# Optimization experiments

Hardware: AMD Instinct MI355X
Metric: run time of the kernel (lower is better)

The kernel has to match this reference:

```python
import jax, jax.numpy as jnp
import numpy as np

E = 8            # n_expert
K = 2            # n_expert_per_token
C = 2048         # n_embd
I = 1408         # moe_intermediate_size
IS = I * 2       # shared expert intermediate (n_shared_expert=2)
B, T = 2, 2048


def setup_inputs() -> dict:
    key = jax.random.key(0)
    ks = jax.random.split(key, 9)
    s = 0.02
    return {
        "x": jax.random.normal(ks[0], (B, T, C), dtype=jnp.float32),
        "gate_w": jax.random.normal(ks[1], (E, C), dtype=jnp.float32) * s,
        # expert MLP weights, torch Linear convention (out_features, in_features)
        "w1": jax.random.normal(ks[2], (E, I, C), dtype=jnp.float32) * s,  # fc_1
        "w2": jax.random.normal(ks[3], (E, I, C), dtype=jnp.float32) * s,  # fc_2
        "w3": jax.random.normal(ks[4], (E, C, I), dtype=jnp.float32) * s,  # proj
        # shared expert
        "sw1": jax.random.normal(ks[5], (IS, C), dtype=jnp.float32) * s,
        "sw2": jax.random.normal(ks[6], (IS, C), dtype=jnp.float32) * s,
        "sw3": jax.random.normal(ks[7], (C, IS), dtype=jnp.float32) * s,
    }


def reference(x, gate_w, w1, w2, w3, sw1, sw2, sw3):
    Bq, Tq, Cq = x.shape
    xf = x.reshape(-1, Cq)  # [N, C], N = B*T

    # top-k routing: softmax in fp32, then top-k probs per token
    logits = xf @ gate_w.T                                   # [N, E]
    probs = jax.nn.softmax(logits.astype(jnp.float32), axis=-1)
    topk_p, topk_i = jax.lax.top_k(probs, K)                 # [N, K]
    # combine weights: comb[n, e] = sum_k topk_p[n,k] * (topk_i[n,k] == e)
    comb = (jax.nn.one_hot(topk_i, E, dtype=jnp.float32)
            * topk_p[..., None]).sum(axis=1).astype(x.dtype)  # [N, E]

    # per-expert gated-SiLU MLP (batched over experts via einsum)
    h1 = jnp.einsum('nc,eic->eni', xf, w1)                   # [E, N, I]
    h2 = jnp.einsum('nc,eic->eni', xf, w2)                   # [E, N, I]
    h = jax.nn.silu(h1) * h2
    eo = jnp.einsum('eni,eci->enc', h, w3)                   # [E, N, C]

    # weighted scatter-combine
    y = jnp.einsum('enc,ne->nc', eo, comb).reshape(Bq, Tq, Cq)

    # shared expert on the residual input
    sh = (jax.nn.silu(xf @ sw1.T) * (xf @ sw2.T)) @ sw3.T    # [N, C]
    return y + sh.reshape(Bq, Tq, Cq)
```

## Files before the change

### kernel.cpp

```cpp
#include <hip/hip_runtime.h>
#include <stdint.h>

#define N_TOK 4096
#define CDIM  2048
#define NEXP  8
#define IDIM  1408
#define ISDIM 2816
#define CAP   2048
#define ICAT  2816
#define SCAT  5632

typedef __attribute__((ext_vector_type(8))) short bf16x8;
typedef __attribute__((ext_vector_type(4))) float f32x4;

#define GLOAD16(gp, lp) __builtin_amdgcn_global_load_lds( \
    (const __attribute__((address_space(1))) void*)(gp),  \
    (__attribute__((address_space(3))) void*)(lp), 16, 0, 0)

__device__ __forceinline__ unsigned short f2bf(float f) {
  union { float f; unsigned u; } c; c.f = f;
  return (unsigned short)((c.u + 0x7FFFu + ((c.u >> 16) & 1u)) >> 16);
}
__device__ __forceinline__ float bf2f(unsigned short h) {
  union { unsigned u; float f; } c; c.u = (unsigned)h << 16;
  return c.f;
}

__device__ __forceinline__ int xcd_swizzle(int orig, int nwg) {
  int q = nwg >> 3, r = nwg & 7;
  int xcd = orig & 7, idx = orig >> 3;
  return (xcd < r ? xcd * (q + 1) : r * (q + 1) + (xcd - r) * q) + idx;
}

__global__ __launch_bounds__(256) void cvt_all(
    const float* __restrict__ x, const float* __restrict__ w1,
    const float* __restrict__ w2, const float* __restrict__ w3,
    const float* __restrict__ sw1, const float* __restrict__ sw2,
    const float* __restrict__ sw3,
    unsigned short* __restrict__ xb, unsigned short* __restrict__ wcat,
    unsigned short* __restrict__ w3b, unsigned short* __restrict__ swcat,
    unsigned short* __restrict__ sw3b) {
  const int b = blockIdx.x;
  const int t = threadIdx.x;
  const float* src;
  unsigned short* dst;
  if (b < 4096) {
    src = x + (size_t)b * 2048;  dst = xb + (size_t)b * 2048;
  } else if (b < 15360) {
    size_t o = (size_t)(b - 4096) * 2048;  src = w3 + o;  dst = w3b + o;
  } else if (b < 18176) {
    size_t o = (size_t)(b - 15360) * 2048; src = sw3 + o; dst = sw3b + o;
  } else if (b < 40704) {
    int g = b - 18176;
    int e = g / 2816, r = g - e * 2816;
    int dr;
    if (r < 1408) { src = w1 + ((size_t)e * 1408 + r) * 2048; dr = (r >> 7) * 256 + (r & 127); }
    else { int r2 = r - 1408; src = w2 + ((size_t)e * 1408 + r2) * 2048; dr = (r2 >> 7) * 256 + 128 + (r2 & 127); }
    dst = wcat + ((size_t)e * ICAT + dr) * 2048;
  } else {
    int g = b - 40704;
    int dr;
    if (g < 2816) {
      int zn = g >= 1408, rr = g - zn * 1408;
      src = sw1 + (size_t)g * 2048;
      dr = zn * 2816 + (rr >> 7) * 256 + (rr & 127);
    } else {
      int r = g - 2816;
      int zn = r >= 1408, rr = r - zn * 1408;
      src = sw2 + (size_t)r * 2048;
      dr = zn * 2816 + (rr >> 7) * 256 + 128 + (rr & 127);
    }
    dst = swcat + (size_t)dr * 2048;
  }
  size_t i = (size_t)t * 8;
  float4 v0 = *(const float4*)(src + i);
  float4 v1 = *(const float4*)(src + i + 4);
  bf16x8 o;
  o[0] = (short)f2bf(v0.x); o[1] = (short)f2bf(v0.y);
  o[2] = (short)f2bf(v0.z); o[3] = (short)f2bf(v0.w);
  o[4] = (short)f2bf(v1.x); o[5] = (short)f2bf(v1.y);
  o[6] = (short)f2bf(v1.z); o[7] = (short)f2bf(v1.w);
  *(bf16x8*)(dst + i) = o;
}

__global__ __launch_bounds__(64) void routing_kernel(
    const float* __restrict__ x, const float* __restrict__ gw,
    int* __restrict__ counts, int* __restrict__ list,
    int* __restrict__ slot_of, float* __restrict__ wts) {
  const int n = blockIdx.x;
  const int lane = threadIdx.x;
  const float* xr = x + (size_t)n * CDIM;
  float s[NEXP];
#pragma unroll
  for (int e = 0; e < NEXP; e++) s[e] = 0.f;
  for (int c = lane; c < CDIM; c += 64) {
    float xv = xr[c];
#pragma unroll
    for (int e = 0; e < NEXP; e++) s[e] += xv * gw[e * CDIM + c];
  }
#pragma unroll
  for (int e = 0; e < NEXP; e++) {
    float v = s[e];
    for (int o = 32; o > 0; o >>= 1) v += __shfl_down(v, o);
    s[e] = v;
  }
  if (lane == 0) {
    float mx = s[0];
#pragma unroll
    for (int e = 1; e < NEXP; e++) mx = fmaxf(mx, s[e]);
    float p[NEXP], sum = 0.f;
#pragma unroll
    for (int e = 0; e < NEXP; e++) { p[e] = __expf(s[e] - mx); sum += p[e]; }
    int i0 = 0;
#pragma unroll
    for (int e = 1; e < NEXP; e++) if (p[e] > p[i0]) i0 = e;
    int i1 = (i0 == 0) ? 1 : 0;
#pragma unroll
    for (int e = 0; e < NEXP; e++) if (e != i0 && p[e] > p[i1]) i1 = e;
    float inv = 1.f / sum;
    int s0 = atomicAdd(&counts[i0], 1);
    int s1 = atomicAdd(&counts[i1], 1);
    if (s0 < CAP) list[i0 * CAP + s0] = n; else s0 = 0;
    if (s1 < CAP) list[i1 * CAP + s1] = n; else s1 = 0;
    slot_of[n * 2]     = i0 * CAP + s0;
    slot_of[n * 2 + 1] = i1 * CAP + s1;
    wts[n * 2]     = p[i0] * inv;
    wts[n * 2 + 1] = p[i1] * inv;
  }
}

template <int PHASE>
__global__ __launch_bounds__(512, 2) void moe_gemm(
    const unsigned short* __restrict__ xb,
    const unsigned short* __restrict__ swcat,
    const unsigned short* __restrict__ wcat,
    unsigned short* __restrict__ hs_out,
    unsigned short* __restrict__ he_out,
    const unsigned short* __restrict__ hs,
    const unsigned short* __restrict__ sw3b,
    const unsigned short* __restrict__ he,
    const unsigned short* __restrict__ w3b,
    float* __restrict__ ysf,
    unsigned short* __restrict__ eo,
    const int* __restrict__ list,
    const int* __restrict__ counts) {
  const int z = blockIdx.z;
  const unsigned short *A, *B;
  unsigned short* O = nullptr;
  float* Of = nullptr;
  int Ka, ldo;
  int cnt = 1 << 30;
  const int* lst = nullptr;
  int Mt, Nt;
  bool gath = false;
  if (PHASE == 1) {
    Mt = 16; Ka = CDIM;
    if (z < 2) {
      Nt = 22;
      A = xb + (size_t)z * 2048 * CDIM;
      B = swcat;
      O = hs_out + (size_t)z * 2048 * ISDIM;
      ldo = ISDIM;
    } else {
      Nt = 11;
      int e = z - 2;
      cnt = counts[e]; if (cnt > CAP) cnt = CAP;
      lst = list + e * CAP;
      gath = true;
      A = xb;
      B = wcat + (size_t)e * ICAT * CDIM;
      O = he_out + (size_t)e * CAP * IDIM;
      ldo = IDIM;
    }
  } else {
    Mt = 16; Nt = 8;
    if (z < 2) {
      Ka = ISDIM;
      A = hs + (size_t)z * 2048 * ISDIM;
      B = sw3b;
      Of = ysf + (size_t)z * 2048 * CDIM;
      ldo = CDIM;
    } else {
      int e = z - 2;
      cnt = counts[e]; if (cnt > CAP) cnt = CAP;
      Ka = IDIM;
      A = he + (size_t)e * CAP * IDIM;
      B = w3b + (size_t)e * CDIM * IDIM;
      O = eo + (size_t)e * CAP * CDIM;
      ldo = CDIM;
    }
  }
  const int nwg = Mt * Nt;
  if ((int)blockIdx.x >= nwg) return;
  const int wg = xcd_swizzle(blockIdx.x, nwg);
  const int mt = wg % Mt, nt = wg / Mt;
  if (mt * 128 >= cnt) return;

  __shared__ __align__(16) char lds[2][24576];

  const int tid = threadIdx.x;
  const int srow = tid >> 2;
  const int c16  = (tid & 3) << 4;
  const int scol = c16 ^ (((srow >> 1) & 3) << 4);
  const char* aS;
  const char* bS[2];
  {
    int ar = mt * 128 + srow;
    if (PHASE == 1 && gath) ar = (ar < cnt) ? lst[ar] : lst[0];
    aS = (const char*)A + (size_t)ar * Ka * 2 + scol;
    bS[0] = (const char*)B + (size_t)(nt * 256 + srow) * Ka * 2 + scol;
    bS[1] = (const char*)B + (size_t)(nt * 256 + 128 + srow) * Ka * 2 + scol;
  }
  auto stage = [&](int buf, int kt) {
    size_t kb = (size_t)kt * 64;
    char* d = &lds[buf][0] + tid * 16;
    GLOAD16(aS + kb, d);
    GLOAD16(bS[0] + kb, d + 8192);
    GLOAD16(bS[1] + kb, d + 16384);
  };

  const int lane = tid & 63, wid = tid >> 6;
  const int wr = wid >> 2, wc = wid & 3;
  const int lrow = lane & 15;
  const int klane = (lane >> 4) << 4;
  const int rsw = ((lrow >> 1) & 3) << 4;
  const int aOff = (wr * 64 + lrow) * 64 + (klane ^ rsw);
  const int bOff = 8192 + (wc * 64 + lrow) * 64 + (klane ^ rsw);

  f32x4 acc[4][4];
#pragma unroll
  for (int mf = 0; mf < 4; mf++)
#pragma unroll
    for (int nf = 0; nf < 4; nf++) acc[mf][nf] = (f32x4){0.f, 0.f, 0.f, 0.f};

  stage(0, 0);
  stage(1, 1);

  const int ntk = Ka >> 5;
  for (int t = 0; t < ntk; t++) {
    const char* base = lds[t & 1];
    if (t + 1 < ntk) asm volatile("s_waitcnt vmcnt(3)" ::: "memory");
    else             asm volatile("s_waitcnt vmcnt(0)" ::: "memory");
    __builtin_amdgcn_s_barrier();
    bf16x8 aR[4], bR[4];
#pragma unroll
    for (int i = 0; i < 4; i++) aR[i] = *(const bf16x8*)(base + aOff + i * 1024);
#pragma unroll
    for (int i = 0; i < 4; i++) bR[i] = *(const bf16x8*)(base + bOff + i * 1024);
    asm volatile("s_waitcnt lgkmcnt(0)" ::: "memory");
    __builtin_amdgcn_s_barrier();
    if (t + 2 < ntk) stage(t & 1, t + 2);
    __builtin_amdgcn_s_setprio(1);
#pragma unroll
    for (int nf = 0; nf < 4; nf++)
#pragma unroll
      for (int mf = 0; mf < 4; mf++)
        acc[mf][nf] = __builtin_amdgcn_mfma_f32_16x16x32_bf16(
            aR[mf], bR[nf], acc[mf][nf], 0, 0, 0);
    __builtin_amdgcn_s_setprio(0);
  }

  const int r4 = (lane >> 4) * 4;
  if (PHASE == 1) {
    unsigned short* ldsH = (unsigned short*)&lds[0][0];
    if (wc >= 2) {
      const int cb = (wc - 2) * 64;
#pragma unroll
      for (int mf = 0; mf < 4; mf++)
#pragma unroll
        for (int nf = 0; nf < 4; nf++) {
          int cc = cb + nf * 16 + lrow;
#pragma unroll
          for (int r = 0; r < 4; r++) {
            int rr = wr * 64 + mf * 16 + r4 + r;
            ldsH[rr * 128 + (cc ^ (((rr >> 2) & 7) << 4))] = f2bf(acc[mf][nf][r]);
          }
        }
    }
    __syncthreads();
    if (wc < 2) {
      const int cb = wc * 64;
#pragma unroll
      for (int mf = 0; mf < 4; mf++) {
#pragma unroll
        for (int nf = 0; nf < 4; nf++) {
          int cc = cb + nf * 16 + lrow;
          int col = nt * 128 + cc;
#pragma unroll
          for (int r = 0; r < 4; r++) {
            int rr = wr * 64 + mf * 16 + r4 + r;
            float z1 = acc[mf][nf][r];
            float z2 = bf2f(ldsH[rr * 128 + (cc ^ (((rr >> 2) & 7) << 4))]);
            float gv = z1 / (1.f + __expf(-z1)) * z2;
            O[(size_t)(mt * 128 + rr) * ldo + col] = f2bf(gv);
          }
        }
      }
    }
  } else {
    const int rowb = mt * 128 + wr * 64;
    const int colb = nt * 256 + wc * 64;
#pragma unroll
    for (int mf = 0; mf < 4; mf++) {
      int row0 = rowb + mf * 16 + r4;
#pragma unroll
      for (int nf = 0; nf < 4; nf++) {
        int col = colb + nf * 16 + lrow;
#pragma unroll
        for (int r = 0; r < 4; r++) {
          if (z < 2)
            Of[(size_t)(row0 + r) * ldo + col] = acc[mf][nf][r];
          else
            O[(size_t)(row0 + r) * ldo + col] = f2bf(acc[mf][nf][r]);
        }
      }
    }
  }
}

__global__ __launch_bounds__(256) void combine_kernel(
    float* __restrict__ y, const float* __restrict__ ysf,
    const unsigned short* __restrict__ eo,
    const int* __restrict__ slot_of, const float* __restrict__ wts) {
  int idx = blockIdx.x * 256 + threadIdx.x;
  int n = idx >> 9;
  int c = (idx & 511) * 4;
  float4 v = *(const float4*)(ysf + (size_t)n * CDIM + c);
#pragma unroll
  for (int k = 0; k < 2; k++) {
    int slot = slot_of[n * 2 + k];
    float w = wts[n * 2 + k];
    ushort4 h = *(const ushort4*)(eo + (size_t)slot * CDIM + c);
    v.x += w * bf2f(h.x);
    v.y += w * bf2f(h.y);
    v.z += w * bf2f(h.z);
    v.w += w * bf2f(h.w);
  }
  *(float4*)(y + (size_t)n * CDIM + c) = v;
}

extern "C" void kernel_launch(void* const* d_in, const int* in_sizes, int n_in,
                              void* d_out, int out_size, void* d_ws, size_t ws_size,
                              hipStream_t stream) {
  const float* x   = (const float*)d_in[0];
  const float* gw  = (const float*)d_in[1];
  const float* w1  = (const float*)d_in[2];
  const float* w2  = (const float*)d_in[3];
  const float* w3  = (const float*)d_in[4];
  const float* sw1 = (const float*)d_in[5];
  const float* sw2 = (const float*)d_in[6];
  const float* sw3 = (const float*)d_in[7];
  float* y = (float*)d_out;

  char* ws = (char*)d_ws;
  size_t off = 0;
  auto alloc = [&](size_t b) -> void* {
    void* p = ws + off;
    off += (b + 255) & ~(size_t)255;
    return p;
  };
  unsigned short* xb    = (unsigned short*)alloc((size_t)N_TOK * CDIM * 2);
  unsigned short* wcat  = (unsigned short*)alloc((size_t)NEXP * ICAT * CDIM * 2);
  unsigned short* w3b   = (unsigned short*)alloc((size_t)NEXP * CDIM * IDIM * 2);
  unsigned short* swcat = (unsigned short*)alloc((size_t)SCAT * CDIM * 2);
  unsigned short* sw3b  = (unsigned short*)alloc((size_t)CDIM * ISDIM * 2);
  unsigned short* hs    = (unsigned short*)alloc((size_t)N_TOK * ISDIM * 2);
  unsigned short* he    = (unsigned short*)alloc((size_t)NEXP * CAP * IDIM * 2);
  float*          ysf   = (float*)alloc((size_t)N_TOK * CDIM * 4);
  int*   counts  = (int*)alloc(NEXP * 4);
  int*   list    = (int*)alloc((size_t)NEXP * CAP * 4);
  int*   slot_of = (int*)alloc((size_t)N_TOK * 2 * 4);
  float* wtsb    = (float*)alloc((size_t)N_TOK * 2 * 4);
  unsigned short* eoB = wcat;

  hipMemsetAsync(counts, 0, NEXP * 4, stream);
  routing_kernel<<<N_TOK, 64, 0, stream>>>(x, gw, counts, list, slot_of, wtsb);

  cvt_all<<<46336, 256, 0, stream>>>(x, w1, w2, w3, sw1, sw2, sw3,
                                     xb, wcat, w3b, swcat, sw3b);

  moe_gemm<1><<<dim3(352, 1, 10), 512, 0, stream>>>(
      xb, swcat, wcat, hs, he, hs, sw3b, he, w3b, ysf, eoB, list, counts);

  moe_gemm<2><<<dim3(128, 1, 10), 512, 0, stream>>>(
      xb, swcat, wcat, hs, he, hs, sw3b, he, w3b, ysf, eoB, list, counts);

  combine_kernel<<<(N_TOK * (CDIM / 4)) / 256, 256, 0, stream>>>(y, ysf, eoB, slot_of, wtsb);
}
```

Measured before the change: 633.2 us.

## Enlarge GEMM tiles to 256x256 with triple-buffered LDS pipeline

Doubles the M tile of both MoE GEMM phases from 128 to 256 rows, so each workgroup holds 8x4 MFMA accumulators per wave and reuses each B tile across twice as many rows. It also switches LDS staging from double to triple buffering, which removes the second barrier per k-step, and splits the shared-expert phase-1 work into four z-slices instead of two. This halves the number of A/B tile reloads and the sync overhead. In exchange it drops the occupancy hint from 2 to 1 workgroup per CU, raises register pressure, uses 96KB of LDS, and launches fewer workgroups, which may underfill the GPU, especially for lightly loaded experts.

```diff
diff --git a/kernel.cpp b/kernel.cpp
--- a/kernel.cpp
+++ b/kernel.cpp
@@ -130,7 +130,7 @@
 }
 
 template <int PHASE>
-__global__ __launch_bounds__(512, 2) void moe_gemm(
+__global__ __launch_bounds__(512) void moe_gemm(
     const unsigned short* __restrict__ xb,
     const unsigned short* __restrict__ swcat,
     const unsigned short* __restrict__ wcat,
@@ -154,16 +154,15 @@
   int Mt, Nt;
   bool gath = false;
   if (PHASE == 1) {
-    Mt = 16; Ka = CDIM;
-    if (z < 2) {
-      Nt = 22;
-      A = xb + (size_t)z * 2048 * CDIM;
-      B = swcat;
-      O = hs_out + (size_t)z * 2048 * ISDIM;
+    Mt = 8; Nt = 11; Ka = CDIM;
+    if (z < 4) {
+      int zm = z >> 1, zn = z & 1;
+      A = xb + (size_t)zm * 2048 * CDIM;
+      B = swcat + (size_t)zn * 2816 * CDIM;
+      O = hs_out + (size_t)zm * 2048 * ISDIM + (size_t)zn * 1408;
       ldo = ISDIM;
     } else {
-      Nt = 11;
-      int e = z - 2;
+      int e = z - 4;
       cnt = counts[e]; if (cnt > CAP) cnt = CAP;
       lst = list + e * CAP;
       gath = true;
@@ -173,7 +172,7 @@
       ldo = IDIM;
     }
   } else {
-    Mt = 16; Nt = 8;
+    Mt = 8; Nt = 8;
     if (z < 2) {
       Ka = ISDIM;
       A = hs + (size_t)z * 2048 * ISDIM;
@@ -190,33 +189,36 @@
       ldo = CDIM;
     }
   }
-  const int nwg = Mt * Nt;
-  if ((int)blockIdx.x >= nwg) return;
-  const int wg = xcd_swizzle(blockIdx.x, nwg);
+  const int wg = xcd_swizzle(blockIdx.x, Mt * Nt);
   const int mt = wg % Mt, nt = wg / Mt;
-  if (mt * 128 >= cnt) return;
-
-  __shared__ __align__(16) char lds[2][24576];
+  if (mt * 256 >= cnt) return;
+
+  __shared__ __align__(16) char lds[3][32768];
 
   const int tid = threadIdx.x;
   const int srow = tid >> 2;
   const int c16  = (tid & 3) << 4;
   const int scol = c16 ^ (((srow >> 1) & 3) << 4);
-  const char* aS;
-  const char* bS[2];
+  const char *aS0, *aS1, *bS0, *bS1;
   {
-    int ar = mt * 128 + srow;
-    if (PHASE == 1 && gath) ar = (ar < cnt) ? lst[ar] : lst[0];
-    aS = (const char*)A + (size_t)ar * Ka * 2 + scol;
-    bS[0] = (const char*)B + (size_t)(nt * 256 + srow) * Ka * 2 + scol;
-    bS[1] = (const char*)B + (size_t)(nt * 256 + 128 + srow) * Ka * 2 + scol;
+    int ar0 = mt * 256 + srow;
+    int ar1 = mt * 256 + 128 + srow;
+    if (PHASE == 1 && gath) {
+      ar0 = (ar0 < cnt) ? lst[ar0] : lst[0];
+      ar1 = (ar1 < cnt) ? lst[ar1] : lst[0];
+    }
+    aS0 = (const char*)A + (size_t)ar0 * Ka * 2 + scol;
+    aS1 = (const char*)A + (size_t)ar1 * Ka * 2 + scol;
+    bS0 = (const char*)B + (size_t)(nt * 256 + srow) * Ka * 2 + scol;
+    bS1 = (const char*)B + (size_t)(nt * 256 + 128 + srow) * Ka * 2 + scol;
   }
   auto stage = [&](int buf, int kt) {
     size_t kb = (size_t)kt * 64;
     char* d = &lds[buf][0] + tid * 16;
-    GLOAD16(aS + kb, d);
-    GLOAD16(bS[0] + kb, d + 8192);
-    GLOAD16(bS[1] + kb, d + 16384);
+    GLOAD16(aS0 + kb, d);
+    GLOAD16(aS1 + kb, d + 8192);
+    GLOAD16(bS0 + kb, d + 16384);
+    GLOAD16(bS1 + kb, d + 24576);
   };
 
   const int lane = tid & 63, wid = tid >> 6;
@@ -224,12 +226,12 @@
   const int lrow = lane & 15;
   const int klane = (lane >> 4) << 4;
   const int rsw = ((lrow >> 1) & 3) << 4;
-  const int aOff = (wr * 64 + lrow) * 64 + (klane ^ rsw);
-  const int bOff = 8192 + (wc * 64 + lrow) * 64 + (klane ^ rsw);
-
-  f32x4 acc[4][4];
-#pragma unroll
-  for (int mf = 0; mf < 4; mf++)
+  const int aOff = (wr * 128 + lrow) * 64 + (klane ^ rsw);
+  const int bOff = 16384 + (wc * 64 + lrow) * 64 + (klane ^ rsw);
+
+  f32x4 acc[8][4];
+#pragma unroll
+  for (int mf = 0; mf < 8; mf++)
 #pragma unroll
     for (int nf = 0; nf < 4; nf++) acc[mf][nf] = (f32x4){0.f, 0.f, 0.f, 0.f};
 
@@ -237,42 +239,44 @@
   stage(1, 1);
 
   const int ntk = Ka >> 5;
+  int cur = 0, nx2 = 2;
   for (int t = 0; t < ntk; t++) {
-    const char* base = lds[t & 1];
-    if (t + 1 < ntk) asm volatile("s_waitcnt vmcnt(3)" ::: "memory");
+    if (t + 1 < ntk) asm volatile("s_waitcnt vmcnt(4)" ::: "memory");
     else             asm volatile("s_waitcnt vmcnt(0)" ::: "memory");
     __builtin_amdgcn_s_barrier();
-    bf16x8 aR[4], bR[4];
-#pragma unroll
-    for (int i = 0; i < 4; i++) aR[i] = *(const bf16x8*)(base + aOff + i * 1024);
+    const char* base = lds[cur];
+    bf16x8 aR[8], bR[4];
+#pragma unroll
+    for (int i = 0; i < 8; i++) aR[i] = *(const bf16x8*)(base + aOff + i * 1024);
 #pragma unroll
     for (int i = 0; i < 4; i++) bR[i] = *(const bf16x8*)(base + bOff + i * 1024);
-    asm volatile("s_waitcnt lgkmcnt(0)" ::: "memory");
-    __builtin_amdgcn_s_barrier();
-    if (t + 2 < ntk) stage(t & 1, t + 2);
+    if (t + 2 < ntk) stage(nx2, t + 2);
     __builtin_amdgcn_s_setprio(1);
 #pragma unroll
     for (int nf = 0; nf < 4; nf++)
 #pragma unroll
-      for (int mf = 0; mf < 4; mf++)
+      for (int mf = 0; mf < 8; mf++)
         acc[mf][nf] = __builtin_amdgcn_mfma_f32_16x16x32_bf16(
             aR[mf], bR[nf], acc[mf][nf], 0, 0, 0);
     __builtin_amdgcn_s_setprio(0);
+    cur = (cur == 2) ? 0 : cur + 1;
+    nx2 = (nx2 == 2) ? 0 : nx2 + 1;
   }
 
   const int r4 = (lane >> 4) * 4;
   if (PHASE == 1) {
+    __syncthreads();
     unsigned short* ldsH = (unsigned short*)&lds[0][0];
     if (wc >= 2) {
       const int cb = (wc - 2) * 64;
 #pragma unroll
-      for (int mf = 0; mf < 4; mf++)
+      for (int mf = 0; mf < 8; mf++)
 #pragma unroll
         for (int nf = 0; nf < 4; nf++) {
           int cc = cb + nf * 16 + lrow;
 #pragma unroll
           for (int r = 0; r < 4; r++) {
-            int rr = wr * 64 + mf * 16 + r4 + r;
+            int rr = wr * 128 + mf * 16 + r4 + r;
             ldsH[rr * 128 + (cc ^ (((rr >> 2) & 7) << 4))] = f2bf(acc[mf][nf][r]);
           }
         }
@@ -281,27 +285,27 @@
     if (wc < 2) {
       const int cb = wc * 64;
 #pragma unroll
-      for (int mf = 0; mf < 4; mf++) {
+      for (int mf = 0; mf < 8; mf++) {
 #pragma unroll
         for (int nf = 0; nf < 4; nf++) {
           int cc = cb + nf * 16 + lrow;
           int col = nt * 128 + cc;
 #pragma unroll
           for (int r = 0; r < 4; r++) {
-            int rr = wr * 64 + mf * 16 + r4 + r;
+            int rr = wr * 128 + mf * 16 + r4 + r;
             float z1 = acc[mf][nf][r];
             float z2 = bf2f(ldsH[rr * 128 + (cc ^ (((rr >> 2) & 7) << 4))]);
             float gv = z1 / (1.f + __expf(-z1)) * z2;
-            O[(size_t)(mt * 128 + rr) * ldo + col] = f2bf(gv);
+            O[(size_t)(mt * 256 + rr) * ldo + col] = f2bf(gv);
           }
         }
       }
     }
   } else {
-    const int rowb = mt * 128 + wr * 64;
+    const int rowb = mt * 256 + wr * 128;
     const int colb = nt * 256 + wc * 64;
 #pragma unroll
-    for (int mf = 0; mf < 4; mf++) {
+    for (int mf = 0; mf < 8; mf++) {
       int row0 = rowb + mf * 16 + r4;
 #pragma unroll
       for (int nf = 0; nf < 4; nf++) {
@@ -379,10 +383,10 @@
   cvt_all<<<46336, 256, 0, stream>>>(x, w1, w2, w3, sw1, sw2, sw3,
                                      xb, wcat, w3b, swcat, sw3b);
 
-  moe_gemm<1><<<dim3(352, 1, 10), 512, 0, stream>>>(
+  moe_gemm<1><<<dim3(88, 1, 12), 512, 0, stream>>>(
       xb, swcat, wcat, hs, he, hs, sw3b, he, w3b, ysf, eoB, list, counts);
 
-  moe_gemm<2><<<dim3(128, 1, 10), 512, 0, stream>>>(
+  moe_gemm<2><<<dim3(64, 1, 10), 512, 0, stream>>>(
       xb, swcat, wcat, hs, he, hs, sw3b, he, w3b, ysf, eoB, list, counts);
 
   combine_kernel<<<(N_TOK * (CDIM / 4)) / 256, 256, 0, stream>>>(y, ysf, eoB, slot_of, wtsb);
```

New measurement: 596.5 us. -5.8%, faster.
